# Optimization experiments

Hardware: AMD Instinct MI355X
Metric: run time of the kernel (lower is better)

## Reference

```python
import jax, jax.numpy as jnp
import numpy as np

BLOCK = 128
QMAX = 127.0


def act_quant(x2d):
    # Per (row, 128-wide block) symmetric int8 quantization.
    # x2d: [M, K] -> q int8-valued [M, K], scales [M, K//BLOCK]
    M, K = x2d.shape
    xb = x2d.reshape(M, K // BLOCK, BLOCK)
    s = jnp.max(jnp.abs(xb), axis=-1) / QMAX            # [M, K//BLOCK]
    s = jnp.maximum(s, 1e-12)
    q = jnp.clip(jnp.round(xb / s[..., None]), -128.0, 127.0)
    return q, s  # q kept in fp32 (exact small ints)


def weight_quant(w):
    # w: [N, K] -> q [N, K], scales [N//BLOCK, K//BLOCK]
    N, K = w.shape
    wb = w.reshape(N // BLOCK, BLOCK, K // BLOCK, BLOCK)
    s = jnp.max(jnp.abs(wb), axis=(1, 3)) / QMAX        # [N//BLOCK, K//BLOCK]
    s = jnp.maximum(s, 1e-12)
    q = jnp.clip(jnp.round(wb / s[:, None, :, None]), -128.0, 127.0)
    return q.reshape(N, K), s


def setup_inputs() -> dict:
    key = jax.random.key(0)
    k1, k2, k3 = jax.random.split(key, 3)
    x = jax.random.normal(k1, (4, 2048, 4096), dtype=jnp.float32)
    weight = jax.random.normal(k2, (4096, 4096), dtype=jnp.float32) * 0.02
    bias = jax.random.normal(k3, (4096,), dtype=jnp.float32) * 0.02
    return {"x": x, "weight": weight, "bias": bias}


def reference(x, weight, bias):
    # Int8Linear.forward: block-quantize activation, int8 GEMM with
    # grouped dequant scales (equivalent to dequantize-then-matmul), add bias.
    orig_shape = x.shape
    K = weight.shape[1]
    N = weight.shape[0]
    x2d = x.reshape(-1, K)                              # [M, K]
    M = x2d.shape[0]

    xq, xs = act_quant(x2d)                             # [M,Kb,128], [M,Kb]
    wq, ws = weight_quant(weight)                       # [N,K],     [Nb,Kb]

    # Dequantize (exact factorization of the scaled int8 GEMM):
    # out[m,n] = sum_kb xs[m,kb]*ws[nb,kb] * sum_c xq[m,kb,c]*wq[n,kb,c]
    x_dq = (xq * xs[..., None]).reshape(M, K)
    wqb = wq.reshape(N // BLOCK, BLOCK, K // BLOCK, BLOCK)
    w_dq = (wqb * ws[:, None, :, None]).reshape(N, K)

    out = x_dq @ w_dq.T + bias                          # [M, N]
    return out.reshape(orig_shape[:-1] + (N,))
```

## Files before the change

kernel.cpp:

```cpp
#include <hip/hip_runtime.h>
#include <stdint.h>

#define K_DIM 4096
#define N_DIM 4096
#define KB    32
#define QMAXF 127.0f

typedef int v4i __attribute__((ext_vector_type(4)));

__device__ __forceinline__ void async_copy16(void* lds, const void* gptr) {
    __builtin_amdgcn_global_load_lds(
        (__attribute__((address_space(1))) void*)gptr,
        (__attribute__((address_space(3))) void*)lds, 16, 0, 0);
}

__global__ __launch_bounds__(256) void act_quant_kernel(
    const float* __restrict__ x, int8_t* __restrict__ xq,
    float* __restrict__ xs_t, int M)
{
    const int m = blockIdx.x;
    const int t = threadIdx.x;
    const float* xrow = x + (size_t)m * K_DIM;
    int8_t* qrow = xq + (size_t)m * K_DIM;

#pragma unroll
    for (int p = 0; p < 4; ++p) {
        const int base = p * 1024 + t * 4;
        float4 v = *(const float4*)(xrow + base);
        float a = fmaxf(fmaxf(fabsf(v.x), fabsf(v.y)), fmaxf(fabsf(v.z), fabsf(v.w)));
#pragma unroll
        for (int off = 1; off < 32; off <<= 1)
            a = fmaxf(a, __shfl_xor(a, off, 64));
        const float s = fmaxf(a / QMAXF, 1e-12f);
        float q0 = fminf(fmaxf(rintf(v.x / s), -128.f), 127.f);
        float q1 = fminf(fmaxf(rintf(v.y / s), -128.f), 127.f);
        float q2 = fminf(fmaxf(rintf(v.z / s), -128.f), 127.f);
        float q3 = fminf(fmaxf(rintf(v.w / s), -128.f), 127.f);
        char4 pk;
        pk.x = (char)(int)q0; pk.y = (char)(int)q1;
        pk.z = (char)(int)q2; pk.w = (char)(int)q3;
        *(char4*)(qrow + base) = pk;
        if ((t & 31) == 0) {
            const int g = base >> 7;
            xs_t[(size_t)g * M + m] = s;
        }
    }
}

__global__ __launch_bounds__(256) void weight_quant_kernel(
    const float* __restrict__ w, int8_t* __restrict__ wq, float* __restrict__ ws)
{
    const int nb = blockIdx.x >> 5;
    const int kb = blockIdx.x & 31;
    const int t  = threadIdx.x;
    const int n0 = nb * 128, k0 = kb * 128;

    float4 vals[16];
    float a = 0.f;
#pragma unroll
    for (int ii = 0; ii < 16; ++ii) {
        const int e = ii * 1024 + t * 4;
        const int row = e >> 7, col = e & 127;
        float4 v = *(const float4*)(w + (size_t)(n0 + row) * K_DIM + k0 + col);
        vals[ii] = v;
        a = fmaxf(a, fmaxf(fmaxf(fabsf(v.x), fabsf(v.y)), fmaxf(fabsf(v.z), fabsf(v.w))));
    }
#pragma unroll
    for (int off = 1; off < 64; off <<= 1)
        a = fmaxf(a, __shfl_xor(a, off, 64));
    __shared__ float wred[4];
    if ((t & 63) == 0) wred[t >> 6] = a;
    __syncthreads();
    a = fmaxf(fmaxf(wred[0], wred[1]), fmaxf(wred[2], wred[3]));
    const float s = fmaxf(a / QMAXF, 1e-12f);
    if (t == 0) ws[nb * KB + kb] = s;

#pragma unroll
    for (int ii = 0; ii < 16; ++ii) {
        const int e = ii * 1024 + t * 4;
        const int row = e >> 7, col = e & 127;
        float4 v = vals[ii];
        char4 pk;
        pk.x = (char)(int)fminf(fmaxf(rintf(v.x / s), -128.f), 127.f);
        pk.y = (char)(int)fminf(fmaxf(rintf(v.y / s), -128.f), 127.f);
        pk.z = (char)(int)fminf(fmaxf(rintf(v.z / s), -128.f), 127.f);
        pk.w = (char)(int)fminf(fmaxf(rintf(v.w / s), -128.f), 127.f);
        *(char4*)(wq + (size_t)(n0 + row) * K_DIM + k0 + col) = pk;
    }
}

__global__ __launch_bounds__(256, 2) void gemm_kernel(
    const int8_t* __restrict__ xq, const int8_t* __restrict__ wq,
    const float* __restrict__ xs_t, const float* __restrict__ ws,
    const float* __restrict__ bias, float* __restrict__ out, int M)
{
    __shared__ __align__(16) int8_t As[128 * 128];
    __shared__ __align__(16) int8_t Bs[128 * 128];
    __shared__ __align__(16) float  xs_s[KB * 128];
    __shared__ float ws_s[KB];

    const int t    = threadIdx.x;
    const int lane = t & 63;
    const int wave = t >> 6;
    const int nb   = blockIdx.x;
    const int n0   = nb * 128;
    const int m0   = blockIdx.y * 128;

#pragma unroll
    for (int i = 0; i < 4; ++i) {
        const int idx = t * 4 + i * 1024;
        const int kbi = idx >> 7, r = idx & 127;
        *(float4*)&xs_s[idx] = *(const float4*)&xs_t[(size_t)kbi * M + m0 + r];
    }
    if (t < KB) ws_s[t] = ws[nb * KB + t];

    const int wm    = (wave >> 1) * 64;
    const int wn    = (wave & 1) * 64;
    const int frow  = lane & 15;
    const int kq    = (lane >> 4) * 16;
    const int quad4 = (lane >> 4) * 4;

    float4 facc[4][4] = {};

    float bj[4];
#pragma unroll
    for (int j = 0; j < 4; ++j) bj[j] = bias[n0 + wn + j * 16 + frow];

    for (int kb = 0; kb < KB; ++kb) {
        __syncthreads();
        const int8_t* Ag = xq + (size_t)m0 * K_DIM + kb * 128;
        const int8_t* Bg = wq + (size_t)n0 * K_DIM + kb * 128;
#pragma unroll
        for (int it = 0; it < 4; ++it) {
            const int ci  = it * 256 + t;
            const int row = ci >> 3, ch = ci & 7;
            void* la = (void*)&As[(it * 256 + wave * 64) * 16];
            void* lb = (void*)&Bs[(it * 256 + wave * 64) * 16];
            async_copy16(la, Ag + (size_t)row * K_DIM + ch * 16);
            async_copy16(lb, Bg + (size_t)row * K_DIM + ch * 16);
        }
        __syncthreads();

        v4i a0[4], a1[4], b0[4], b1[4];
#pragma unroll
        for (int i = 0; i < 4; ++i) {
            a0[i] = *(const v4i*)&As[(wm + i * 16 + frow) * 128 + kq];
            a1[i] = *(const v4i*)&As[(wm + i * 16 + frow) * 128 + 64 + kq];
            b0[i] = *(const v4i*)&Bs[(wn + i * 16 + frow) * 128 + kq];
            b1[i] = *(const v4i*)&Bs[(wn + i * 16 + frow) * 128 + 64 + kq];
        }
        const float wskb = ws_s[kb];
#pragma unroll
        for (int i = 0; i < 4; ++i) {
            float4 xs4 = *(const float4*)&xs_s[kb * 128 + wm + i * 16 + quad4];
            const float s0 = xs4.x * wskb, s1 = xs4.y * wskb;
            const float s2 = xs4.z * wskb, s3 = xs4.w * wskb;
#pragma unroll
            for (int j = 0; j < 4; ++j) {
                v4i d = __builtin_amdgcn_mfma_i32_16x16x64_i8(a0[i], b0[j], (v4i){0, 0, 0, 0}, 0, 0, 0);
                d = __builtin_amdgcn_mfma_i32_16x16x64_i8(a1[i], b1[j], d, 0, 0, 0);
                facc[i][j].x += (float)d[0] * s0;
                facc[i][j].y += (float)d[1] * s1;
                facc[i][j].z += (float)d[2] * s2;
                facc[i][j].w += (float)d[3] * s3;
            }
        }
    }

#pragma unroll
    for (int i = 0; i < 4; ++i) {
#pragma unroll
        for (int r = 0; r < 4; ++r) {
            const int row = m0 + wm + i * 16 + quad4 + r;
            float* orow = out + (size_t)row * N_DIM + n0 + wn + frow;
#pragma unroll
            for (int j = 0; j < 4; ++j)
                orow[j * 16] = ((const float*)&facc[i][j])[r] + bj[j];
        }
    }
}

extern "C" void kernel_launch(void* const* d_in, const int* in_sizes, int n_in,
                              void* d_out, int out_size, void* d_ws, size_t ws_size,
                              hipStream_t stream)
{
    const float* x    = (const float*)d_in[0];
    const float* w    = (const float*)d_in[1];
    const float* bias = (const float*)d_in[2];
    float* out = (float*)d_out;
    const int M = in_sizes[0] / K_DIM;

    int8_t* xq  = (int8_t*)d_ws;
    int8_t* wqp = xq + (size_t)M * K_DIM;
    float*  xst = (float*)(wqp + (size_t)N_DIM * K_DIM);
    float*  wsp = xst + (size_t)KB * M;

    act_quant_kernel<<<M, 256, 0, stream>>>(x, xq, xst, M);
    weight_quant_kernel<<<(N_DIM / 128) * KB, 256, 0, stream>>>(w, wqp, wsp);
    gemm_kernel<<<dim3(N_DIM / 128, M / 128), 256, 0, stream>>>(
        xq, wqp, xst, wsp, bias, out, M);
}
```

Measured before the change: 485.1 us.

## Swizzle int8 GEMM LDS tiles, raise occupancy, use reciprocal in quant

Applies an XOR swizzle to the 16-byte chunk placement of the A and B tiles in shared memory so the MFMA fragment reads hit different LDS banks, with matching swizzled read offsets. Also raises the GEMM launch bound from 2 to 3 blocks per CU to allow more latency hiding, at the cost of register pressure. The quantization kernels now multiply by a precomputed reciprocal scale instead of dividing, which may change rounding slightly at ties.

```diff
diff --git a/kernel.cpp b/kernel.cpp
--- a/kernel.cpp
+++ b/kernel.cpp
@@ -32,10 +32,11 @@
         for (int off = 1; off < 32; off <<= 1)
             a = fmaxf(a, __shfl_xor(a, off, 64));
         const float s = fmaxf(a / QMAXF, 1e-12f);
-        float q0 = fminf(fmaxf(rintf(v.x / s), -128.f), 127.f);
-        float q1 = fminf(fmaxf(rintf(v.y / s), -128.f), 127.f);
-        float q2 = fminf(fmaxf(rintf(v.z / s), -128.f), 127.f);
-        float q3 = fminf(fmaxf(rintf(v.w / s), -128.f), 127.f);
+        const float inv = 1.0f / s;
+        float q0 = fminf(fmaxf(rintf(v.x * inv), -128.f), 127.f);
+        float q1 = fminf(fmaxf(rintf(v.y * inv), -128.f), 127.f);
+        float q2 = fminf(fmaxf(rintf(v.z * inv), -128.f), 127.f);
+        float q3 = fminf(fmaxf(rintf(v.w * inv), -128.f), 127.f);
         char4 pk;
         pk.x = (char)(int)q0; pk.y = (char)(int)q1;
         pk.z = (char)(int)q2; pk.w = (char)(int)q3;
@@ -73,6 +74,7 @@
     __syncthreads();
     a = fmaxf(fmaxf(wred[0], wred[1]), fmaxf(wred[2], wred[3]));
     const float s = fmaxf(a / QMAXF, 1e-12f);
+    const float inv = 1.0f / s;
     if (t == 0) ws[nb * KB + kb] = s;
 
 #pragma unroll
@@ -81,15 +83,15 @@
         const int row = e >> 7, col = e & 127;
         float4 v = vals[ii];
         char4 pk;
-        pk.x = (char)(int)fminf(fmaxf(rintf(v.x / s), -128.f), 127.f);
-        pk.y = (char)(int)fminf(fmaxf(rintf(v.y / s), -128.f), 127.f);
-        pk.z = (char)(int)fminf(fmaxf(rintf(v.z / s), -128.f), 127.f);
-        pk.w = (char)(int)fminf(fmaxf(rintf(v.w / s), -128.f), 127.f);
+        pk.x = (char)(int)fminf(fmaxf(rintf(v.x * inv), -128.f), 127.f);
+        pk.y = (char)(int)fminf(fmaxf(rintf(v.y * inv), -128.f), 127.f);
+        pk.z = (char)(int)fminf(fmaxf(rintf(v.z * inv), -128.f), 127.f);
+        pk.w = (char)(int)fminf(fmaxf(rintf(v.w * inv), -128.f), 127.f);
         *(char4*)(wq + (size_t)(n0 + row) * K_DIM + k0 + col) = pk;
     }
 }
 
-__global__ __launch_bounds__(256, 2) void gemm_kernel(
+__global__ __launch_bounds__(256, 3) void gemm_kernel(
     const int8_t* __restrict__ xq, const int8_t* __restrict__ wq,
     const float* __restrict__ xs_t, const float* __restrict__ ws,
     const float* __restrict__ bias, float* __restrict__ out, int M)
@@ -117,8 +119,9 @@
     const int wm    = (wave >> 1) * 64;
     const int wn    = (wave & 1) * 64;
     const int frow  = lane & 15;
-    const int kq    = (lane >> 4) * 16;
-    const int quad4 = (lane >> 4) * 4;
+    const int q     = lane >> 4;
+    const int quad4 = q * 4;
+    const int sw0   = ((q ^ (frow & 7)) * 16);
 
     float4 facc[4][4] = {};
 
@@ -133,21 +136,22 @@
 #pragma unroll
         for (int it = 0; it < 4; ++it) {
             const int ci  = it * 256 + t;
-            const int row = ci >> 3, ch = ci & 7;
+            const int row = ci >> 3;
+            const int c   = (ci & 7) ^ (row & 7);
             void* la = (void*)&As[(it * 256 + wave * 64) * 16];
             void* lb = (void*)&Bs[(it * 256 + wave * 64) * 16];
-            async_copy16(la, Ag + (size_t)row * K_DIM + ch * 16);
-            async_copy16(lb, Bg + (size_t)row * K_DIM + ch * 16);
+            async_copy16(la, Ag + (size_t)row * K_DIM + c * 16);
+            async_copy16(lb, Bg + (size_t)row * K_DIM + c * 16);
         }
         __syncthreads();
 
         v4i a0[4], a1[4], b0[4], b1[4];
 #pragma unroll
         for (int i = 0; i < 4; ++i) {
-            a0[i] = *(const v4i*)&As[(wm + i * 16 + frow) * 128 + kq];
-            a1[i] = *(const v4i*)&As[(wm + i * 16 + frow) * 128 + 64 + kq];
-            b0[i] = *(const v4i*)&Bs[(wn + i * 16 + frow) * 128 + kq];
-            b1[i] = *(const v4i*)&Bs[(wn + i * 16 + frow) * 128 + 64 + kq];
+            a0[i] = *(const v4i*)&As[(wm + i * 16 + frow) * 128 + sw0];
+            a1[i] = *(const v4i*)&As[(wm + i * 16 + frow) * 128 + (sw0 ^ 64)];
+            b0[i] = *(const v4i*)&Bs[(wn + i * 16 + frow) * 128 + sw0];
+            b1[i] = *(const v4i*)&Bs[(wn + i * 16 + frow) * 128 + (sw0 ^ 64)];
         }
         const float wskb = ws_s[kb];
 #pragma unroll
```

New measurement: 446.1 us. 1.09x faster.
